# Kernel tuning notes

Measured on AMD Instinct MI355X. Metric: run time of the kernel, lower is better.

The kernel has to match this reference:

```python
import jax, jax.numpy as jnp
import numpy as np

D_MODEL = 192
EXPAND = 2
D_INNER = EXPAND * D_MODEL          # 384
HEADDIM = 64
NHEADS = D_INNER // HEADDIM         # 6
DSTATE = 64
CONV_DIM = D_INNER + DSTATE         # 448
D_IN_PROJ = 2 * D_INNER + DSTATE    # 832
BATCH, Hh, Ww = 8, 96, 96
SCALE = HEADDIM ** -0.5


def dwconv(x, w, b, pad):
    # x: [B, C, H, W], w: [C, 1, k, k] depthwise conv
    y = jax.lax.conv_general_dilated(
        x, w, window_strides=(1, 1), padding=[(pad, pad), (pad, pad)],
        dimension_numbers=('NCHW', 'OIHW', 'NCHW'),
        feature_group_count=x.shape[1])
    return y + b[None, :, None, None]


def setup_inputs() -> dict:
    key = jax.random.key(0)
    ks = jax.random.split(key, 8)
    s = 0.02
    return {
        'u': jax.random.normal(ks[0], (BATCH, Hh * Ww, D_MODEL), jnp.float32),
        'W_in': jax.random.normal(ks[1], (D_MODEL, D_IN_PROJ), jnp.float32) * s,
        'conv_w': jax.random.normal(ks[2], (CONV_DIM, 1, 3, 3), jnp.float32) * s,
        'conv_b': jnp.zeros((CONV_DIM,), jnp.float32),
        'lc_dw_w': jax.random.normal(ks[3], (D_INNER, 1, 5, 5), jnp.float32) * s,
        'lc_dw_b': jnp.zeros((D_INNER,), jnp.float32),
        'lc_pw_w': jax.random.normal(ks[4], (D_INNER, D_INNER), jnp.float32) * s,
        'lc_pw_b': jnp.zeros((D_INNER,), jnp.float32),
        'D': jnp.ones((NHEADS,), jnp.float32),
        'ln_g': jnp.ones((D_INNER,), jnp.float32),
        'ln_b': jnp.zeros((D_INNER,), jnp.float32),
        'W_out': jax.random.normal(ks[5], (D_INNER, D_MODEL), jnp.float32) * s,
        'H': Hh,
        'W': Ww,
    }


def reference(u, W_in, conv_w, conv_b, lc_dw_w, lc_dw_b, lc_pw_w, lc_pw_b,
              D, ln_g, ln_b, W_out, H, W):
    b, L, _ = u.shape
    # in_proj (no bias) and split
    zxB = u @ W_in                                   # [b, L, 832]
    z, xB = zxB[..., :D_INNER], zxB[..., D_INNER:]   # [b,L,384], [b,L,448]
    # depthwise 3x3 conv over the spatial grid + SiLU
    xB_im = xB.reshape(b, H, W, CONV_DIM).transpose(0, 3, 1, 2)
    xB_im = jax.nn.silu(dwconv(xB_im, conv_w, conv_b, 1))
    xB = xB_im.transpose(0, 2, 3, 1).reshape(b, L, CONV_DIM)
    x, Bm = xB[..., :D_INNER], xB[..., D_INNER:]     # [b,L,384], [b,L,64]

    # ---- dpa ----
    # sigmoid-normalized routing weights over dstate (shared across heads)
    Ksig = jax.nn.sigmoid(Bm)                        # [b, L, s]
    K_soft = Ksig / (Ksig.sum(-1, keepdims=True) + 1e-6)
    V = x.reshape(b, L, NHEADS, HEADDIM).transpose(0, 2, 1, 3)  # [b,h,l,d]
    # local conv: 5x5 depthwise + 1x1 pointwise
    x_im = x.reshape(b, H, W, D_INNER).transpose(0, 3, 1, 2)    # [b,(h d),H,W]
    x_loc = dwconv(x_im, lc_dw_w, lc_dw_b, 2)
    x_loc = jnp.einsum('oc,bchw->bohw', lc_pw_w, x_loc) + lc_pw_b[None, :, None, None]
    Vs = x_loc.reshape(b, NHEADS, HEADDIM, L).transpose(0, 1, 3, 2)  # [b,h,l,d]

    proto = jnp.einsum('bls,bhld->bhsd', K_soft, Vs)            # class prototypes
    scores = jnp.einsum('bhsd,bhld->bhsl', proto, Vs) * SCALE
    attn = jax.nn.softmax(scores, axis=-1)                      # softmax over l
    refined = jnp.einsum('bhsl,bhld->bhsd', attn, Vs)
    fine = jnp.einsum('bls,bhsd->bhld', K_soft, refined)
    y = fine + V * D[None, :, None, None]                       # D residual
    y = y.transpose(0, 2, 1, 3).reshape(b, L, D_INNER)

    # LayerNorm, gate by z, out_proj
    mu = y.mean(-1, keepdims=True)
    var = y.var(-1, keepdims=True)
    y = (y - mu) * jax.lax.rsqrt(var + 1e-5) * ln_g + ln_b
    y = y * z
    return y @ W_out
```

## Files before the change

### kernel.cpp

```cpp
#include <hip/hip_runtime.h>

#define B_ 8
#define H_ 96
#define W_ 96
#define L_ (H_*W_)
#define M_ (B_*L_)
#define DM 192
#define DI 384
#define DS 64
#define CD 448
#define NH 6
#define HD 64
#define SCALE_ 0.125f
#define LSPLIT 16

typedef unsigned short bfu;
typedef __attribute__((ext_vector_type(8))) short bf16x8;
typedef __attribute__((ext_vector_type(8))) unsigned short u16x8;
typedef __attribute__((ext_vector_type(4))) float f32x4;

__device__ __forceinline__ float sigm(float x){ return 1.f/(1.f+__expf(-x)); }
__device__ __forceinline__ float b2f(bfu h){ return __uint_as_float(((unsigned)h)<<16); }
__device__ __forceinline__ bfu f2b(float f){
  unsigned x = __float_as_uint(f);
  return (bfu)((x + 0x7fffu + ((x>>16)&1u)) >> 16);
}
__device__ __forceinline__ float4 ld4(const float* p){ return *(const float4*)p; }
__device__ __forceinline__ float4 ld4(const bfu* p){
  ushort4 u = *(const ushort4*)p;
  return make_float4(b2f(u.x), b2f(u.y), b2f(u.z), b2f(u.w));
}
__device__ __forceinline__ void stage8(const float* src, bfu* dst){
  float4 f0 = *(const float4*)(src), f1 = *(const float4*)(src+4);
  ushort4 a; a.x=f2b(f0.x); a.y=f2b(f0.y); a.z=f2b(f0.z); a.w=f2b(f0.w);
  ushort4 b; b.x=f2b(f1.x); b.y=f2b(f1.y); b.z=f2b(f1.z); b.w=f2b(f1.w);
  *(ushort4*)dst = a; *(ushort4*)(dst+4) = b;
}
__device__ __forceinline__ void stel(float* p, float v){ *p = v; }
__device__ __forceinline__ void stel(bfu* p, float v){ *p = f2b(v); }

__device__ __forceinline__ void gload16(const bfu* g, bfu* l){
  __builtin_amdgcn_global_load_lds(
      (const __attribute__((address_space(1))) unsigned int*)(const void*)g,
      (__attribute__((address_space(3))) unsigned int*)(void*)l, 16, 0, 0);
}

#define SWZ(r, sg) ((((sg) ^ ((r)&7)) << 3))
#define SWZE(r, c) (SWZ(r, (c)>>3) + ((c)&7))

template<bool BIAS, class TC0, class TC1>
__global__ __launch_bounds__(256) void gemm_mfma(
    const bfu* __restrict__ A, const bfu* __restrict__ Bw,
    const float* __restrict__ bias,
    TC0* __restrict__ C0, TC1* __restrict__ C1,
    int K, int splitN, int ldc0, int ldc1,
    long sA, long sB, long sC)
{
  __shared__ alignas(16) bfu As[128][64];
  __shared__ alignas(16) bfu Bs[64][64];
  const int tid = threadIdx.x;
  const int gx = gridDim.x;
  int flat = blockIdx.y*gx + blockIdx.x;
  const int cpx = (gx*gridDim.y) >> 3;
  flat = (flat & 7)*cpx + (flat >> 3);
  const int n0 = (flat % gx)*64, m0 = (flat / gx)*128, zb = blockIdx.z;
  A  += (long)zb*sA;
  Bw += (long)zb*sB;
  const int wave = tid>>6, lane = tid&63;
  const int wr = wave>>1, wc = wave&1;
  const int lr = lane&15, lk = lane>>4;
  f32x4 acc[4][2];
  #pragma unroll
  for (int mr=0;mr<4;++mr)
    #pragma unroll
    for (int nr=0;nr<2;++nr){ acc[mr][nr][0]=0.f; acc[mr][nr][1]=0.f; acc[mr][nr][2]=0.f; acc[mr][nr][3]=0.f; }
  for (int k0 = 0; k0 < K; k0 += 64) {
    #pragma unroll
    for (int i = 0; i < 4; ++i) {
      int seg = i*256 + tid;
      int r = seg>>3, t = seg&7;
      gload16(A + (long)(m0+r)*K + k0 + ((t ^ (r&7))<<3), &As[0][0] + seg*8);
    }
    #pragma unroll
    for (int i = 0; i < 2; ++i) {
      int seg = i*256 + tid;
      int r = seg>>3, t = seg&7;
      gload16(Bw + (long)(n0+r)*K + k0 + ((t ^ (r&7))<<3), &Bs[0][0] + seg*8);
    }
    __syncthreads();
    #pragma unroll
    for (int ks = 0; ks < 2; ++ks) {
      bf16x8 af[4], bfr[2];
      #pragma unroll
      for (int mr=0; mr<4; ++mr){ int r = wr*64+mr*16+lr; af[mr]  = *(const bf16x8*)&As[r][SWZ(r, ks*4+lk)]; }
      #pragma unroll
      for (int nr=0; nr<2; ++nr){ int r = wc*32+nr*16+lr; bfr[nr] = *(const bf16x8*)&Bs[r][SWZ(r, ks*4+lk)]; }
      #pragma unroll
      for (int mr=0; mr<4; ++mr)
        #pragma unroll
        for (int nr=0; nr<2; ++nr)
          acc[mr][nr] = __builtin_amdgcn_mfma_f32_16x16x32_bf16(af[mr], bfr[nr], acc[mr][nr], 0,0,0);
    }
    __syncthreads();
  }
  #pragma unroll
  for (int mr=0; mr<4; ++mr) {
    #pragma unroll
    for (int nr=0; nr<2; ++nr) {
      const int col = n0 + wc*32 + nr*16 + lr;
      const float badd = BIAS ? bias[col] : 0.f;
      #pragma unroll
      for (int i=0;i<4;++i) {
        const int row = m0 + wr*64 + mr*16 + lk*4 + i;
        const float v = acc[mr][nr][i] + badd;
        if (col < splitN) stel(C0 + (long)zb*sC + (long)row*ldc0 + col, v);
        else              stel(C1 + (long)row*ldc1 + (col - splitN), v);
      }
    }
  }
}

__global__ __launch_bounds__(256) void conv_u(
    const float* __restrict__ u, bfu* __restrict__ ub)
{
  int i = blockIdx.x*256 + threadIdx.x;
  if (i >= M_*DM/8) return;
  stage8(u + (size_t)i*8, ub + (size_t)i*8);
}

__global__ __launch_bounds__(256) void prep_w(
    const float* __restrict__ W_in, const float* __restrict__ pw_w,
    const float* __restrict__ W_out,
    bfu* __restrict__ Wt_in, bfu* __restrict__ pw_bf, bfu* __restrict__ Wt_out)
{
  int i = blockIdx.x*256 + threadIdx.x;
  const int n1 = 832*192, n2 = n1 + 384*384, n3 = n2 + 192*384;
  if (i < n1)      { int n=i/192, k=i%192; Wt_in[i]  = f2b(W_in[k*832+n]); }
  else if (i < n2) { int j=i-n1;           pw_bf[j]  = f2b(pw_w[j]); }
  else if (i < n3) { int j=i-n2; int n=j/384, k=j%384; Wt_out[j] = f2b(W_out[k*192+n]); }
}

__global__ __launch_bounds__(256) void conv3x3_t(
    const bfu* __restrict__ xB, const float* __restrict__ cw,
    const float* __restrict__ cb, bfu* __restrict__ out)
{
  const int tile = blockIdx.x, c0 = blockIdx.y*8, b = blockIdx.z;
  const int h0 = (tile/6)*16, w0 = (tile%6)*16;
  __shared__ alignas(16) bfu tl[18][18][8];
  __shared__ float wl[8][9];
  const int tid = threadIdx.x;
  if (tid < 72) wl[tid/9][tid%9] = cw[(c0 + tid/9)*9 + tid%9];
  for (int i = tid; i < 324; i += 256) {
    int y = i/18, x = i%18;
    int gh = h0+y-1, gw = w0+x-1;
    uint4 v = make_uint4(0,0,0,0);
    if ((unsigned)gh < 96u && (unsigned)gw < 96u)
      v = *(const uint4*)(xB + ((long)(b*L_ + gh*96+gw))*CD + c0);
    *(uint4*)&tl[y][x][0] = v;
  }
  __syncthreads();
  const int px = tid & 15, py = tid >> 4;
  float a[8];
  #pragma unroll
  for (int j=0;j<8;++j) a[j] = cb[c0+j];
  #pragma unroll
  for (int dh=0; dh<3; ++dh)
    #pragma unroll
    for (int dw=0; dw<3; ++dw) {
      uint4 r = *(const uint4*)&tl[py+dh][px+dw][0];
      int t = dh*3+dw;
      a[0] += __uint_as_float(r.x<<16)        * wl[0][t];
      a[1] += __uint_as_float(r.x&0xffff0000u)* wl[1][t];
      a[2] += __uint_as_float(r.y<<16)        * wl[2][t];
      a[3] += __uint_as_float(r.y&0xffff0000u)* wl[3][t];
      a[4] += __uint_as_float(r.z<<16)        * wl[4][t];
      a[5] += __uint_as_float(r.z&0xffff0000u)* wl[5][t];
      a[6] += __uint_as_float(r.w<<16)        * wl[6][t];
      a[7] += __uint_as_float(r.w&0xffff0000u)* wl[7][t];
    }
  #pragma unroll
  for (int j=0;j<8;++j) a[j] = a[j]*sigm(a[j]);
  uint4 o;
  o.x = (unsigned)f2b(a[0]) | ((unsigned)f2b(a[1])<<16);
  o.y = (unsigned)f2b(a[2]) | ((unsigned)f2b(a[3])<<16);
  o.z = (unsigned)f2b(a[4]) | ((unsigned)f2b(a[5])<<16);
  o.w = (unsigned)f2b(a[6]) | ((unsigned)f2b(a[7])<<16);
  *(uint4*)(out + ((long)(b*L_ + (h0+py)*96 + (w0+px)))*CD + c0) = o;
}

__global__ __launch_bounds__(256) void conv5x5_t(
    const bfu* __restrict__ xin, const float* __restrict__ cw,
    const float* __restrict__ cb, bfu* __restrict__ out)
{
  const int tile = blockIdx.x, c0 = blockIdx.y*8, b = blockIdx.z;
  const int h0 = (tile/6)*16, w0 = (tile%6)*16;
  __shared__ alignas(16) bfu tl[20][20][8];
  __shared__ float wl[8][25];
  const int tid = threadIdx.x;
  if (tid < 200) wl[tid/25][tid%25] = cw[(c0 + tid/25)*25 + tid%25];
  for (int i = tid; i < 400; i += 256) {
    int y = i/20, x = i%20;
    int gh = h0+y-2, gw = w0+x-2;
    uint4 v = make_uint4(0,0,0,0);
    if ((unsigned)gh < 96u && (unsigned)gw < 96u)
      v = *(const uint4*)(xin + ((long)(b*L_ + gh*96+gw))*CD + c0);
    *(uint4*)&tl[y][x][0] = v;
  }
  __syncthreads();
  const int px = tid & 15, py = tid >> 4;
  float a[8];
  #pragma unroll
  for (int j=0;j<8;++j) a[j] = cb[c0+j];
  #pragma unroll
  for (int dh=0; dh<5; ++dh)
    #pragma unroll
    for (int dw=0; dw<5; ++dw) {
      uint4 r = *(const uint4*)&tl[py+dh][px+dw][0];
      int t = dh*5+dw;
      a[0] += __uint_as_float(r.x<<16)        * wl[0][t];
      a[1] += __uint_as_float(r.x&0xffff0000u)* wl[1][t];
      a[2] += __uint_as_float(r.y<<16)        * wl[2][t];
      a[3] += __uint_as_float(r.y&0xffff0000u)* wl[3][t];
      a[4] += __uint_as_float(r.z<<16)        * wl[4][t];
      a[5] += __uint_as_float(r.z&0xffff0000u)* wl[5][t];
      a[6] += __uint_as_float(r.w<<16)        * wl[6][t];
      a[7] += __uint_as_float(r.w&0xffff0000u)* wl[7][t];
    }
  uint4 o;
  o.x = (unsigned)f2b(a[0]) | ((unsigned)f2b(a[1])<<16);
  o.y = (unsigned)f2b(a[2]) | ((unsigned)f2b(a[3])<<16);
  o.z = (unsigned)f2b(a[4]) | ((unsigned)f2b(a[5])<<16);
  o.w = (unsigned)f2b(a[6]) | ((unsigned)f2b(a[7])<<16);
  *(uint4*)(out + ((long)(b*L_ + (h0+py)*96 + (w0+px)))*DI + c0) = o;
}

__global__ __launch_bounds__(256) void ksoft_kernel(
    const bfu* __restrict__ xB2, bfu* __restrict__ Ksoft)
{
  int p = blockIdx.x * 4 + (threadIdx.x >> 6);
  int lane = threadIdx.x & 63;
  float v = b2f(xB2[(long)p * CD + DI + lane]);
  float k = sigm(v);
  float s = k;
  #pragma unroll
  for (int o = 32; o; o >>= 1) s += __shfl_xor(s, o);
  Ksoft[((long)p << 6) + lane] = f2b(k / (s + 1e-6f));
}

__global__ __launch_bounds__(256) void proto_mfma(
    const bfu* __restrict__ Ksf, const bfu* __restrict__ Vs, float* __restrict__ part)
{
  const int ch = blockIdx.x, bh = blockIdx.y;
  const int b = bh / NH, hh = bh % NH;
  __shared__ alignas(16) bfu Kst[64][72];
  __shared__ alignas(16) bfu Vtt[64][72];
  const int tid = threadIdx.x;
  const int wave = tid>>6, lane = tid&63;
  const int wr = wave>>1, wc = wave&1;
  const int lr = lane&15, lk = lane>>4;
  f32x4 acc[2][2];
  #pragma unroll
  for (int mr=0;mr<2;++mr)
    #pragma unroll
    for (int nr=0;nr<2;++nr){ acc[mr][nr][0]=0.f; acc[mr][nr][1]=0.f; acc[mr][nr][2]=0.f; acc[mr][nr][3]=0.f; }
  const int lbeg = ch * (L_/LSPLIT);
  for (int l0 = lbeg; l0 < lbeg + L_/LSPLIT; l0 += 64) {
    __syncthreads();
    #pragma unroll
    for (int i=0;i<2;++i) {
      const int li = tid&63, sg = (tid>>6) + i*4;
      const long lrow = (long)b*L_ + l0 + li;
      u16x8 kv = *(const u16x8*)(Ksf + (lrow<<6) + sg*8);
      u16x8 vv = *(const u16x8*)(Vs + lrow*DI + hh*HD + sg*8);
      #pragma unroll
      for (int j=0;j<8;++j) {
        int r = sg*8+j;
        Kst[r][SWZE(r, li)] = kv[j];
        Vtt[r][SWZE(r, li)] = vv[j];
      }
    }
    __syncthreads();
    #pragma unroll
    for (int ks=0; ks<2; ++ks) {
      bf16x8 af[2], bfr[2];
      #pragma unroll
      for (int mr=0;mr<2;++mr){ int r = wr*32+mr*16+lr; af[mr]  = *(const bf16x8*)&Kst[r][SWZ(r, ks*4+lk)]; }
      #pragma unroll
      for (int nr=0;nr<2;++nr){ int r = wc*32+nr*16+lr; bfr[nr] = *(const bf16x8*)&Vtt[r][SWZ(r, ks*4+lk)]; }
      #pragma unroll
      for (int mr=0;mr<2;++mr)
        #pragma unroll
        for (int nr=0;nr<2;++nr)
          acc[mr][nr] = __builtin_amdgcn_mfma_f32_16x16x32_bf16(af[mr], bfr[nr], acc[mr][nr], 0,0,0);
    }
  }
  float* dst = part + ((long)bh*LSPLIT + ch) * 4096;
  #pragma unroll
  for (int mr=0;mr<2;++mr)
    #pragma unroll
    for (int nr=0;nr<2;++nr)
      #pragma unroll
      for (int i=0;i<4;++i) {
        int row = wr*32+mr*16+lk*4+i, col = wc*32+nr*16+lr;
        dst[row*64+col] = acc[mr][nr][i];
      }
}

__global__ __launch_bounds__(256) void reduce_proto(
    const float* __restrict__ part, bfu* __restrict__ proto)
{
  int idx = blockIdx.x * 256 + threadIdx.x;
  int bh = idx >> 12, sd = idx & 4095;
  const float* p = part + ((long)bh*LSPLIT)*4096 + sd;
  float s = 0.f;
  #pragma unroll
  for (int c = 0; c < LSPLIT; ++c) s += p[c*4096];
  proto[idx] = f2b(s);
}

__global__ __launch_bounds__(256) void flashpv_mfma(
    const bfu* __restrict__ proto, const bfu* __restrict__ Vs,
    float* __restrict__ pacc_part, float* __restrict__ dsum_part)
{
  const int ch = blockIdx.x, bh = blockIdx.y;
  const int b = bh / NH, hh = bh % NH;
  __shared__ alignas(16) bfu Pt[64][72];
  __shared__ alignas(16) bfu Vt[64][72];
  __shared__ alignas(16) bfu Vtt[64][72];
  __shared__ alignas(16) bfu Ptl[64][72];
  __shared__ float dsh[2][64];
  const int tid = threadIdx.x;
  const int wave = tid>>6, lane = tid&63;
  const int wr = wave>>1, wc = wave&1;
  const int lr = lane&15, lk = lane>>4;
  {
    const bfu* src = proto + ((long)bh<<12);
    #pragma unroll
    for (int i=0;i<2;++i) {
      const int li = tid&63, sg = (tid>>6) + i*4;
      *(uint4*)&Pt[li][SWZ(li, sg)] = *(const uint4*)(src + li*64 + sg*8);
    }
  }
  f32x4 pacc[2][2];
  #pragma unroll
  for (int mr=0;mr<2;++mr)
    #pragma unroll
    for (int nr=0;nr<2;++nr){ pacc[mr][nr][0]=0.f; pacc[mr][nr][1]=0.f; pacc[mr][nr][2]=0.f; pacc[mr][nr][3]=0.f; }
  float ds[8] = {};
  const int lbeg = ch * (L_/LSPLIT);
  for (int l0 = lbeg; l0 < lbeg + L_/LSPLIT; l0 += 64) {
    __syncthreads();
    #pragma unroll
    for (int i=0;i<2;++i) {
      const int li = tid&63, sg = (tid>>6) + i*4;
      u16x8 vv = *(const u16x8*)(Vs + ((long)b*L_ + l0 + li)*DI + hh*HD + sg*8);
      *(u16x8*)&Vt[li][SWZ(li, sg)] = vv;
      #pragma unroll
      for (int j=0;j<8;++j) { int r = sg*8+j; Vtt[r][SWZE(r, li)] = vv[j]; }
    }
    __syncthreads();
    f32x4 sacc[2][2];
    #pragma unroll
    for (int mr=0;mr<2;++mr)
      #pragma unroll
      for (int nr=0;nr<2;++nr){ sacc[mr][nr][0]=0.f; sacc[mr][nr][1]=0.f; sacc[mr][nr][2]=0.f; sacc[mr][nr][3]=0.f; }
    #pragma unroll
    for (int ks=0; ks<2; ++ks) {
      bf16x8 af[2], bfr[2];
      #pragma unroll
      for (int mr=0;mr<2;++mr){ int r = wr*32+mr*16+lr; af[mr]  = *(const bf16x8*)&Pt[r][SWZ(r, ks*4+lk)]; }
      #pragma unroll
      for (int nr=0;nr<2;++nr){ int r = wc*32+nr*16+lr; bfr[nr] = *(const bf16x8*)&Vt[r][SWZ(r, ks*4+lk)]; }
      #pragma unroll
      for (int mr=0;mr<2;++mr)
        #pragma unroll
        for (int nr=0;nr<2;++nr)
          sacc[mr][nr] = __builtin_amdgcn_mfma_f32_16x16x32_bf16(af[mr], bfr[nr], sacc[mr][nr], 0,0,0);
    }
    #pragma unroll
    for (int mr=0;mr<2;++mr)
      #pragma unroll
      for (int nr=0;nr<2;++nr)
        #pragma unroll
        for (int i=0;i<4;++i) {
          int row = wr*32+mr*16+lk*4+i, col = wc*32+nr*16+lr;
          float p = __expf(sacc[mr][nr][i]*SCALE_);
          ds[mr*4+i] += p;
          Ptl[row][SWZE(row, col)] = f2b(p);
        }
    __syncthreads();
    #pragma unroll
    for (int ks=0; ks<2; ++ks) {
      bf16x8 af2[2], bf2[2];
      #pragma unroll
      for (int mr=0;mr<2;++mr){ int r = wr*32+mr*16+lr; af2[mr] = *(const bf16x8*)&Ptl[r][SWZ(r, ks*4+lk)]; }
      #pragma unroll
      for (int nr=0;nr<2;++nr){ int r = wc*32+nr*16+lr; bf2[nr] = *(const bf16x8*)&Vtt[r][SWZ(r, ks*4+lk)]; }
      #pragma unroll
      for (int mr=0;mr<2;++mr)
        #pragma unroll
        for (int nr=0;nr<2;++nr)
          pacc[mr][nr] = __builtin_amdgcn_mfma_f32_16x16x32_bf16(af2[mr], bf2[nr], pacc[mr][nr], 0,0,0);
    }
  }
  float* dst = pacc_part + ((long)bh*LSPLIT + ch) * 4096;
  #pragma unroll
  for (int mr=0;mr<2;++mr)
    #pragma unroll
    for (int nr=0;nr<2;++nr)
      #pragma unroll
      for (int i=0;i<4;++i) {
        int row = wr*32+mr*16+lk*4+i, col = wc*32+nr*16+lr;
        dst[row*64+col] = pacc[mr][nr][i];
      }
  #pragma unroll
  for (int o=1;o<16;o<<=1)
    #pragma unroll
    for (int j=0;j<8;++j) ds[j] += __shfl_xor(ds[j], o);
  if (lr == 0) {
    #pragma unroll
    for (int mr=0;mr<2;++mr)
      #pragma unroll
      for (int i=0;i<4;++i)
        dsh[wc][wr*32+mr*16+lk*4+i] = ds[mr*4+i];
  }
  __syncthreads();
  if (tid < 64)
    dsum_part[((long)bh*LSPLIT + ch)*64 + tid] = dsh[0][tid] + dsh[1][tid];
}

__global__ __launch_bounds__(256) void reduce_R2(
    const float* __restrict__ pacc_part, const float* __restrict__ dsum_part,
    bfu* __restrict__ R2t)
{
  int idx = blockIdx.x * 256 + threadIdx.x;
  int bh = idx >> 12, s = (idx >> 6) & 63, d = idx & 63;
  int b = bh / NH, hh = bh % NH;
  float pa = 0.f, dsv = 0.f;
  #pragma unroll
  for (int c = 0; c < LSPLIT; ++c) {
    pa += pacc_part[((long)bh*LSPLIT + c)*4096 + (s<<6) + d];
    dsv += dsum_part[((long)bh*LSPLIT + c)*64 + s];
  }
  R2t[(((long)b*DI) + hh*HD + d)*64 + s] = f2b(pa / dsv);
}

__global__ __launch_bounds__(128) void ln_kernel(
    const bfu* __restrict__ fine, const bfu* __restrict__ xB2,
    const bfu* __restrict__ z, const float* __restrict__ Dv,
    const float* __restrict__ ln_g, const float* __restrict__ ln_b,
    bfu* __restrict__ yn)
{
  const int p = blockIdx.x;
  const int tid = threadIdx.x;
  __shared__ float sh[2], sh2[2];
  float y[3]; float s = 0.f, ss = 0.f;
  #pragma unroll
  for (int k = 0; k < 3; ++k) {
    int c = tid + (k << 7);
    float f = b2f(fine[(long)p*DI + c]) + b2f(xB2[(long)p*CD + c]) * Dv[c >> 6];
    y[k] = f; s += f; ss += f*f;
  }
  #pragma unroll
  for (int o = 32; o; o >>= 1) { s += __shfl_xor(s, o); ss += __shfl_xor(ss, o); }
  if ((tid & 63) == 0) { sh[tid >> 6] = s; sh2[tid >> 6] = ss; }
  __syncthreads();
  s = sh[0] + sh[1]; ss = sh2[0] + sh2[1];
  float mu = s * (1.f/384.f);
  float var = ss * (1.f/384.f) - mu*mu;
  float rs = rsqrtf(var + 1e-5f);
  #pragma unroll
  for (int k = 0; k < 3; ++k) {
    int c = tid + (k << 7);
    float o2 = (y[k] - mu) * rs * ln_g[c] + ln_b[c];
    yn[(long)p*DI + c] = f2b(o2 * b2f(z[(long)p*DI + c]));
  }
}

extern "C" void kernel_launch(void* const* d_in, const int* in_sizes, int n_in,
                              void* d_out, int out_size, void* d_ws, size_t ws_size,
                              hipStream_t stream) {
  const float* u      = (const float*)d_in[0];
  const float* W_in   = (const float*)d_in[1];
  const float* conv_w = (const float*)d_in[2];
  const float* conv_b = (const float*)d_in[3];
  const float* dw_w   = (const float*)d_in[4];
  const float* dw_b   = (const float*)d_in[5];
  const float* pw_w   = (const float*)d_in[6];
  const float* pw_b   = (const float*)d_in[7];
  const float* Dv     = (const float*)d_in[8];
  const float* ln_g   = (const float*)d_in[9];
  const float* ln_b   = (const float*)d_in[10];
  const float* W_out  = (const float*)d_in[11];
  float* out = (float*)d_out;

  bfu* z_bf = (bfu*)d_out;

  char* ws = (char*)d_ws;
  size_t off = 0;
  bfu* xB_bf   = (bfu*)(ws + off); off += (size_t)M_*CD*2;
  bfu* xB2_bf  = (bfu*)(ws + off); off += (size_t)M_*CD*2;
  bfu* xloc_bf = (bfu*)(ws + off); off += (size_t)M_*DI*2;
  bfu* Vs_bf   = (bfu*)(ws + off); off += (size_t)M_*DI*2;
  bfu* Ksf_bf  = (bfu*)(ws + off); off += (size_t)M_*DS*2;
  bfu* Wt_in   = (bfu*)(ws + off); off += (size_t)832*192*2;
  bfu* pw_bf   = (bfu*)(ws + off); off += (size_t)384*384*2;
  bfu* Wt_out  = (bfu*)(ws + off); off += (size_t)192*384*2;
  bfu* R2t     = (bfu*)(ws + off); off += (size_t)8*DI*64*2;
  bfu* proto_b = (bfu*)(ws + off); off += (size_t)48*4096*2;
  bfu*   u_bf  = xloc_bf;
  float* part  = (float*)xloc_bf;
  float* dsum  = part + (size_t)48*LSPLIT*4096;

  bfu* fine_bf = xB_bf;
  bfu* yn_bf   = xloc_bf;

  prep_w<<<1488, 256, 0, stream>>>(W_in, pw_w, W_out, Wt_in, pw_bf, Wt_out);
  conv_u<<<(M_*DM/8 + 255)/256, 256, 0, stream>>>(u, u_bf);
  gemm_mfma<false,bfu,bfu><<<dim3(13,576,1), 256, 0, stream>>>(
      u_bf, Wt_in, nullptr, z_bf, xB_bf, 192, 384, 384, 448, 0, 0, 0);
  conv3x3_t<<<dim3(36,56,8), 256, 0, stream>>>(xB_bf, conv_w, conv_b, xB2_bf);
  ksoft_kernel<<<M_/4, 256, 0, stream>>>(xB2_bf, Ksf_bf);
  conv5x5_t<<<dim3(36,48,8), 256, 0, stream>>>(xB2_bf, dw_w, dw_b, xloc_bf);
  gemm_mfma<true,bfu,bfu><<<dim3(6,576,1), 256, 0, stream>>>(
      xloc_bf, pw_bf, pw_b, Vs_bf, (bfu*)nullptr, 384, 1<<30, 384, 0, 0, 0, 0);
  proto_mfma<<<dim3(LSPLIT,48), 256, 0, stream>>>(Ksf_bf, Vs_bf, part);
  reduce_proto<<<768, 256, 0, stream>>>(part, proto_b);
  flashpv_mfma<<<dim3(LSPLIT,48), 256, 0, stream>>>(proto_b, Vs_bf, part, dsum);
  reduce_R2<<<768, 256, 0, stream>>>(part, dsum, R2t);
  gemm_mfma<false,bfu,bfu><<<dim3(6,72,8), 256, 0, stream>>>(
      Ksf_bf, R2t, nullptr, fine_bf, (bfu*)nullptr, 64, 1<<30, 384, 0,
      (long)L_*64, (long)DI*64, (long)L_*384);
  ln_kernel<<<M_, 128, 0, stream>>>(fine_bf, xB2_bf, z_bf, Dv, ln_g, ln_b, yn_bf);
  gemm_mfma<false,float,float><<<dim3(3,576,1), 256, 0, stream>>>(
      yn_bf, Wt_out, nullptr, out, (float*)nullptr, 384, 1<<30, 192, 0, 0, 0, 0);
}
```

Baseline: 498.2 us.

## Register-block depthwise convs with packed FMA and vectorize per-row LayerNorm

Replaces the two depthwise conv kernels with one templated kernel. It uses 32x32 spatial tiles, channel-planar shared memory with padding against bank conflicts, and a 4x4 output block per thread that reuses loaded window rows in registers. The inner loop issues v_pk_fma_f32 on two channels at once. This cuts shared-memory reads per FMA and raises FMA throughput, at the cost of more registers and fewer, larger blocks. The LayerNorm kernel now handles one row per wavefront with 8-wide vector loads and shuffle-only reductions, removing the block-level syncthreads and the scalar accesses.

```diff
diff --git a/kernel.cpp b/kernel.cpp
--- a/kernel.cpp
+++ b/kernel.cpp
@@ -18,6 +18,7 @@
 typedef __attribute__((ext_vector_type(8))) short bf16x8;
 typedef __attribute__((ext_vector_type(8))) unsigned short u16x8;
 typedef __attribute__((ext_vector_type(4))) float f32x4;
+typedef __attribute__((ext_vector_type(2))) float f32x2;
 
 __device__ __forceinline__ float sigm(float x){ return 1.f/(1.f+__expf(-x)); }
 __device__ __forceinline__ float b2f(bfu h){ return __uint_as_float(((unsigned)h)<<16); }
@@ -26,10 +27,6 @@
   return (bfu)((x + 0x7fffu + ((x>>16)&1u)) >> 16);
 }
 __device__ __forceinline__ float4 ld4(const float* p){ return *(const float4*)p; }
-__device__ __forceinline__ float4 ld4(const bfu* p){
-  ushort4 u = *(const ushort4*)p;
-  return make_float4(b2f(u.x), b2f(u.y), b2f(u.z), b2f(u.w));
-}
 __device__ __forceinline__ void stage8(const float* src, bfu* dst){
   float4 f0 = *(const float4*)(src), f1 = *(const float4*)(src+4);
   ushort4 a; a.x=f2b(f0.x); a.y=f2b(f0.y); a.z=f2b(f0.z); a.w=f2b(f0.w);
@@ -38,6 +35,10 @@
 }
 __device__ __forceinline__ void stel(float* p, float v){ *p = v; }
 __device__ __forceinline__ void stel(bfu* p, float v){ *p = f2b(v); }
+
+__device__ __forceinline__ void pkfma(f32x2& d, f32x2 a, f32x2 b){
+  asm("v_pk_fma_f32 %0, %1, %2, %0" : "+v"(d) : "v"(a), "v"(b));
+}
 
 __device__ __forceinline__ void gload16(const bfu* g, bfu* l){
   __builtin_amdgcn_global_load_lds(
@@ -140,98 +141,76 @@
   else if (i < n3) { int j=i-n2; int n=j/384, k=j%384; Wt_out[j] = f2b(W_out[k*192+n]); }
 }
 
-__global__ __launch_bounds__(256) void conv3x3_t(
-    const bfu* __restrict__ xB, const float* __restrict__ cw,
+template<int KS, int LDIN, int LDOUT, bool SILU>
+__global__ __launch_bounds__(256) void conv_dw(
+    const bfu* __restrict__ xin, const float* __restrict__ cw,
     const float* __restrict__ cb, bfu* __restrict__ out)
 {
-  const int tile = blockIdx.x, c0 = blockIdx.y*8, b = blockIdx.z;
-  const int h0 = (tile/6)*16, w0 = (tile%6)*16;
-  __shared__ alignas(16) bfu tl[18][18][8];
-  __shared__ float wl[8][9];
+  constexpr int PAD = KS/2;
+  constexpr int WIN = 32 + KS - 1;
+  constexpr int W4  = 4 + KS - 1;
+  constexpr int PLR = WIN*WIN % 32;
+  constexpr int PL  = WIN*WIN + ((PLR <= 20) ? (20 - PLR) : (52 - PLR));
+  __shared__ unsigned pl[4*PL];
   const int tid = threadIdx.x;
-  if (tid < 72) wl[tid/9][tid%9] = cw[(c0 + tid/9)*9 + tid%9];
-  for (int i = tid; i < 324; i += 256) {
-    int y = i/18, x = i%18;
-    int gh = h0+y-1, gw = w0+x-1;
+  const int tile = blockIdx.x, cg = blockIdx.y, b = blockIdx.z;
+  const int h0 = (tile/3)*32, w0 = (tile%3)*32;
+  const int c0 = cg*8;
+  for (int i = tid; i < WIN*WIN; i += 256) {
+    int y = i/WIN, x = i - y*WIN;
+    int gh = h0 + y - PAD, gw = w0 + x - PAD;
     uint4 v = make_uint4(0,0,0,0);
     if ((unsigned)gh < 96u && (unsigned)gw < 96u)
-      v = *(const uint4*)(xB + ((long)(b*L_ + gh*96+gw))*CD + c0);
-    *(uint4*)&tl[y][x][0] = v;
-  }
+      v = *(const uint4*)(xin + ((long)(b*L_ + gh*96+gw))*LDIN + c0);
+    pl[0*PL + i] = v.x; pl[1*PL + i] = v.y; pl[2*PL + i] = v.z; pl[3*PL + i] = v.w;
+  }
+  const int cp = tid & 3, px4 = (tid>>2)&7, py4 = tid>>5;
+  f32x2 w[KS*KS];
+  #pragma unroll
+  for (int t = 0; t < KS*KS; ++t) {
+    w[t][0] = cw[(c0 + 2*cp  )*KS*KS + t];
+    w[t][1] = cw[(c0 + 2*cp+1)*KS*KS + t];
+  }
+  f32x2 bias; bias[0] = cb[c0+2*cp]; bias[1] = cb[c0+2*cp+1];
   __syncthreads();
-  const int px = tid & 15, py = tid >> 4;
-  float a[8];
-  #pragma unroll
-  for (int j=0;j<8;++j) a[j] = cb[c0+j];
-  #pragma unroll
-  for (int dh=0; dh<3; ++dh)
-    #pragma unroll
-    for (int dw=0; dw<3; ++dw) {
-      uint4 r = *(const uint4*)&tl[py+dh][px+dw][0];
-      int t = dh*3+dw;
-      a[0] += __uint_as_float(r.x<<16)        * wl[0][t];
-      a[1] += __uint_as_float(r.x&0xffff0000u)* wl[1][t];
-      a[2] += __uint_as_float(r.y<<16)        * wl[2][t];
-      a[3] += __uint_as_float(r.y&0xffff0000u)* wl[3][t];
-      a[4] += __uint_as_float(r.z<<16)        * wl[4][t];
-      a[5] += __uint_as_float(r.z&0xffff0000u)* wl[5][t];
-      a[6] += __uint_as_float(r.w<<16)        * wl[6][t];
-      a[7] += __uint_as_float(r.w&0xffff0000u)* wl[7][t];
-    }
-  #pragma unroll
-  for (int j=0;j<8;++j) a[j] = a[j]*sigm(a[j]);
-  uint4 o;
-  o.x = (unsigned)f2b(a[0]) | ((unsigned)f2b(a[1])<<16);
-  o.y = (unsigned)f2b(a[2]) | ((unsigned)f2b(a[3])<<16);
-  o.z = (unsigned)f2b(a[4]) | ((unsigned)f2b(a[5])<<16);
-  o.w = (unsigned)f2b(a[6]) | ((unsigned)f2b(a[7])<<16);
-  *(uint4*)(out + ((long)(b*L_ + (h0+py)*96 + (w0+px)))*CD + c0) = o;
-}
-
-__global__ __launch_bounds__(256) void conv5x5_t(
-    const bfu* __restrict__ xin, const float* __restrict__ cw,
-    const float* __restrict__ cb, bfu* __restrict__ out)
-{
-  const int tile = blockIdx.x, c0 = blockIdx.y*8, b = blockIdx.z;
-  const int h0 = (tile/6)*16, w0 = (tile%6)*16;
-  __shared__ alignas(16) bfu tl[20][20][8];
-  __shared__ float wl[8][25];
-  const int tid = threadIdx.x;
-  if (tid < 200) wl[tid/25][tid%25] = cw[(c0 + tid/25)*25 + tid%25];
-  for (int i = tid; i < 400; i += 256) {
-    int y = i/20, x = i%20;
-    int gh = h0+y-2, gw = w0+x-2;
-    uint4 v = make_uint4(0,0,0,0);
-    if ((unsigned)gh < 96u && (unsigned)gw < 96u)
-      v = *(const uint4*)(xin + ((long)(b*L_ + gh*96+gw))*CD + c0);
-    *(uint4*)&tl[y][x][0] = v;
-  }
-  __syncthreads();
-  const int px = tid & 15, py = tid >> 4;
-  float a[8];
-  #pragma unroll
-  for (int j=0;j<8;++j) a[j] = cb[c0+j];
-  #pragma unroll
-  for (int dh=0; dh<5; ++dh)
-    #pragma unroll
-    for (int dw=0; dw<5; ++dw) {
-      uint4 r = *(const uint4*)&tl[py+dh][px+dw][0];
-      int t = dh*5+dw;
-      a[0] += __uint_as_float(r.x<<16)        * wl[0][t];
-      a[1] += __uint_as_float(r.x&0xffff0000u)* wl[1][t];
-      a[2] += __uint_as_float(r.y<<16)        * wl[2][t];
-      a[3] += __uint_as_float(r.y&0xffff0000u)* wl[3][t];
-      a[4] += __uint_as_float(r.z<<16)        * wl[4][t];
-      a[5] += __uint_as_float(r.z&0xffff0000u)* wl[5][t];
-      a[6] += __uint_as_float(r.w<<16)        * wl[6][t];
-      a[7] += __uint_as_float(r.w&0xffff0000u)* wl[7][t];
-    }
-  uint4 o;
-  o.x = (unsigned)f2b(a[0]) | ((unsigned)f2b(a[1])<<16);
-  o.y = (unsigned)f2b(a[2]) | ((unsigned)f2b(a[3])<<16);
-  o.z = (unsigned)f2b(a[4]) | ((unsigned)f2b(a[5])<<16);
-  o.w = (unsigned)f2b(a[6]) | ((unsigned)f2b(a[7])<<16);
-  *(uint4*)(out + ((long)(b*L_ + (h0+py)*96 + (w0+px)))*DI + c0) = o;
+  f32x2 acc[4][4];
+  #pragma unroll
+  for (int oy=0;oy<4;++oy)
+    #pragma unroll
+    for (int ox=0;ox<4;++ox){ acc[oy][ox][0]=0.f; acc[oy][ox][1]=0.f; }
+  const unsigned* mp = pl + cp*PL;
+  const int oy0 = py4*4, ox0 = px4*4;
+  #pragma unroll
+  for (int wy = 0; wy < W4; ++wy) {
+    f32x2 rv[W4];
+    #pragma unroll
+    for (int wx = 0; wx < W4; ++wx) {
+      unsigned uv = mp[(oy0+wy)*WIN + ox0 + wx];
+      rv[wx][0] = __uint_as_float(uv<<16);
+      rv[wx][1] = __uint_as_float(uv & 0xffff0000u);
+    }
+    #pragma unroll
+    for (int oy = 0; oy < 4; ++oy) {
+      if (wy-oy >= 0 && wy-oy < KS) {
+        #pragma unroll
+        for (int ox = 0; ox < 4; ++ox)
+          #pragma unroll
+          for (int tx = 0; tx < KS; ++tx)
+            pkfma(acc[oy][ox], rv[ox+tx], w[(wy-oy)*KS + tx]);
+      }
+    }
+  }
+  #pragma unroll
+  for (int oy = 0; oy < 4; ++oy)
+    #pragma unroll
+    for (int ox = 0; ox < 4; ++ox) {
+      float a0 = acc[oy][ox][0] + bias[0];
+      float a1 = acc[oy][ox][1] + bias[1];
+      if (SILU) { a0 = a0*sigm(a0); a1 = a1*sigm(a1); }
+      unsigned o = (unsigned)f2b(a0) | ((unsigned)f2b(a1)<<16);
+      long p = (long)(b*L_ + (h0+oy0+oy)*96 + (w0+ox0+ox));
+      *(unsigned*)(out + p*LDOUT + c0 + 2*cp) = o;
+    }
 }
 
 __global__ __launch_bounds__(256) void ksoft_kernel(
@@ -445,35 +424,43 @@
   R2t[(((long)b*DI) + hh*HD + d)*64 + s] = f2b(pa / dsv);
 }
 
-__global__ __launch_bounds__(128) void ln_kernel(
+__global__ __launch_bounds__(256) void ln_kernel(
     const bfu* __restrict__ fine, const bfu* __restrict__ xB2,
     const bfu* __restrict__ z, const float* __restrict__ Dv,
     const float* __restrict__ ln_g, const float* __restrict__ ln_b,
     bfu* __restrict__ yn)
 {
-  const int p = blockIdx.x;
-  const int tid = threadIdx.x;
-  __shared__ float sh[2], sh2[2];
-  float y[3]; float s = 0.f, ss = 0.f;
-  #pragma unroll
-  for (int k = 0; k < 3; ++k) {
-    int c = tid + (k << 7);
-    float f = b2f(fine[(long)p*DI + c]) + b2f(xB2[(long)p*CD + c]) * Dv[c >> 6];
-    y[k] = f; s += f; ss += f*f;
+  const int p = blockIdx.x*4 + (threadIdx.x >> 6);
+  const int lane = threadIdx.x & 63;
+  float v[8]; float s = 0.f, ss = 0.f;
+  if (lane < 48) {
+    u16x8 fv = *(const u16x8*)(fine + (long)p*DI + lane*8);
+    u16x8 xv = *(const u16x8*)(xB2 + (long)p*CD + lane*8);
+    const float dv = Dv[lane >> 3];
+    #pragma unroll
+    for (int j=0;j<8;++j) {
+      float f = b2f((bfu)fv[j]) + b2f((bfu)xv[j]) * dv;
+      v[j] = f; s += f; ss += f*f;
+    }
   }
   #pragma unroll
   for (int o = 32; o; o >>= 1) { s += __shfl_xor(s, o); ss += __shfl_xor(ss, o); }
-  if ((tid & 63) == 0) { sh[tid >> 6] = s; sh2[tid >> 6] = ss; }
-  __syncthreads();
-  s = sh[0] + sh[1]; ss = sh2[0] + sh2[1];
   float mu = s * (1.f/384.f);
   float var = ss * (1.f/384.f) - mu*mu;
   float rs = rsqrtf(var + 1e-5f);
-  #pragma unroll
-  for (int k = 0; k < 3; ++k) {
-    int c = tid + (k << 7);
-    float o2 = (y[k] - mu) * rs * ln_g[c] + ln_b[c];
-    yn[(long)p*DI + c] = f2b(o2 * b2f(z[(long)p*DI + c]));
+  if (lane < 48) {
+    u16x8 zv = *(const u16x8*)(z + (long)p*DI + lane*8);
+    float4 g0 = ld4(ln_g + lane*8), g1 = ld4(ln_g + lane*8 + 4);
+    float4 b0 = ld4(ln_b + lane*8), b1 = ld4(ln_b + lane*8 + 4);
+    float g[8] = {g0.x,g0.y,g0.z,g0.w,g1.x,g1.y,g1.z,g1.w};
+    float bb[8] = {b0.x,b0.y,b0.z,b0.w,b1.x,b1.y,b1.z,b1.w};
+    u16x8 ov;
+    #pragma unroll
+    for (int j=0;j<8;++j) {
+      float o2 = (v[j] - mu) * rs * g[j] + bb[j];
+      ov[j] = f2b(o2 * b2f((bfu)zv[j]));
+    }
+    *(u16x8*)(yn + (long)p*DI + lane*8) = ov;
   }
 }
 
@@ -519,9 +506,9 @@
   conv_u<<<(M_*DM/8 + 255)/256, 256, 0, stream>>>(u, u_bf);
   gemm_mfma<false,bfu,bfu><<<dim3(13,576,1), 256, 0, stream>>>(
       u_bf, Wt_in, nullptr, z_bf, xB_bf, 192, 384, 384, 448, 0, 0, 0);
-  conv3x3_t<<<dim3(36,56,8), 256, 0, stream>>>(xB_bf, conv_w, conv_b, xB2_bf);
+  conv_dw<3,CD,CD,true><<<dim3(9,56,8), 256, 0, stream>>>(xB_bf, conv_w, conv_b, xB2_bf);
   ksoft_kernel<<<M_/4, 256, 0, stream>>>(xB2_bf, Ksf_bf);
-  conv5x5_t<<<dim3(36,48,8), 256, 0, stream>>>(xB2_bf, dw_w, dw_b, xloc_bf);
+  conv_dw<5,CD,DI,false><<<dim3(9,48,8), 256, 0, stream>>>(xB2_bf, dw_w, dw_b, xloc_bf);
   gemm_mfma<true,bfu,bfu><<<dim3(6,576,1), 256, 0, stream>>>(
       xloc_bf, pw_bf, pw_b, Vs_bf, (bfu*)nullptr, 384, 1<<30, 384, 0, 0, 0, 0);
   proto_mfma<<<dim3(LSPLIT,48), 256, 0, stream>>>(Ksf_bf, Vs_bf, part);
@@ -531,7 +518,7 @@
   gemm_mfma<false,bfu,bfu><<<dim3(6,72,8), 256, 0, stream>>>(
       Ksf_bf, R2t, nullptr, fine_bf, (bfu*)nullptr, 64, 1<<30, 384, 0,
       (long)L_*64, (long)DI*64, (long)L_*384);
-  ln_kernel<<<M_, 128, 0, stream>>>(fine_bf, xB2_bf, z_bf, Dv, ln_g, ln_b, yn_bf);
+  ln_kernel<<<M_/4, 256, 0, stream>>>(fine_bf, xB2_bf, z_bf, Dv, ln_g, ln_b, yn_bf);
   gemm_mfma<false,float,float><<<dim3(3,576,1), 256, 0, stream>>>(
       yn_bf, Wt_out, nullptr, out, (float*)nullptr, 384, 1<<30, 192, 0, 0, 0, 0);
 }
```

Measured after the change: 593.4 us. +19.1%, slower.
